# Optimization experiments

Hardware: AMD Instinct MI355X
Metric: run time of the kernel (lower is better)

## Reference

```python
import jax, jax.numpy as jnp
import numpy as np

L, K, C, D, E = 4, 3, 512, 512, 512   # layers, kwidth, channels, embed_dim, encoding_dim
T, B, S, V, MAXT = 1024, 16, 512, 32, 1024


def setup_inputs() -> dict:
    key = jax.random.key(0)
    ks = jax.random.split(key, 16)
    n = lambda k, sh, s=0.02: jax.random.normal(k, sh, dtype=jnp.float32) * s
    return {
        "labels": jax.random.randint(ks[0], (T, B), 0, V),
        "enc_seq": jax.random.uniform(ks[1], (S, B, E), dtype=jnp.float32),
        "label_embed_W": n(ks[2], (V, D)),
        "time_embed_W": n(ks[3], (MAXT, D)),
        "conv_glu_w": n(ks[4], (L, C, C, K)),
        "conv_glu_b": jnp.zeros((L, C), jnp.float32),
        "conv_id_w": n(ks[5], (L, C, C, K)),
        "conv_id_b": jnp.zeros((L, C), jnp.float32),
        "res_proj_w": n(ks[6], (L, C, C)),
        "res_proj_b": jnp.zeros((L, C), jnp.float32),
        "inres_w": n(ks[7], (L, C, D)),
        "inres_b": jnp.zeros((L, C), jnp.float32),
        "in2enc_w": n(ks[8], (L, E, C)),
        "in2enc_b": jnp.ones((L, E), jnp.float32),  # positive bias keeps sum-normalizer well conditioned
        "lab2enc_w": n(ks[9], (L, E, D)),
        "lab2enc_b": jnp.zeros((L, E), jnp.float32),
        "enc2in_w": n(ks[10], (L, C, E)),
        "enc2in_b": jnp.zeros((L, C), jnp.float32),
        "out_res_w": n(ks[11], (V, D)),
        "out_res_b": jnp.zeros((V,), jnp.float32),
        "out_proj_w": n(ks[12], (V, C)),
        "out_proj_b": jnp.zeros((V,), jnp.float32),
    }


def causal_conv(x, w, b):
    # x: (T, B, Cin); w: (Cout, Cin, K) -> left-padded (causal) conv, out (T, B, Cout)
    x_ = jnp.transpose(x, (1, 2, 0))  # (B, Cin, T)
    y = jax.lax.conv_general_dilated(
        x_, w, window_strides=(1,), padding=[(w.shape[-1] - 1, 0)],
        dimension_numbers=("NCH", "OIH", "NCH"))
    return jnp.transpose(y, (2, 0, 1)) + b


def reference(labels, enc_seq, label_embed_W, time_embed_W, conv_glu_w, conv_glu_b,
              conv_id_w, conv_id_b, res_proj_w, res_proj_b, inres_w, inres_b,
              in2enc_w, in2enc_b, lab2enc_w, lab2enc_b, enc2in_w, enc2in_b,
              out_res_w, out_res_b, out_proj_w, out_proj_b):
    Tn = labels.shape[0]
    emb = label_embed_W[labels] + time_embed_W[jnp.arange(Tn)][:, None, :]  # (T,B,D)
    h = emb
    for i in range(conv_glu_w.shape[0]):
        x = causal_conv(h, conv_glu_w[i], conv_glu_b[i])
        g = causal_conv(h, conv_id_w[i], conv_id_b[i])
        conv_out = (x * jax.nn.sigmoid(g)
                    + jnp.einsum('tbc,oc->tbo', h, res_proj_w[i]) + res_proj_b[i])
        # attention: dot-product scores normalized by their SUM over encoder axis (no softmax)
        d = (jnp.einsum('tbc,ec->tbe', conv_out, in2enc_w[i]) + in2enc_b[i]
             + jnp.einsum('tbd,ed->tbe', emb, lab2enc_w[i]) + lab2enc_b[i])
        raw = jnp.einsum('tbe,sbe->tsb', d, enc_seq)          # (T,S,B)
        attn = raw / jnp.sum(raw, axis=1, keepdims=True)
        ctx = jnp.einsum('tsb,sbe->tbe', attn, enc_seq)        # (T,B,E)
        ctx_proj = jnp.einsum('tbe,ce->tbc', ctx, enc2in_w[i]) + enc2in_b[i]
        h = conv_out + ctx_proj + jnp.einsum('tbd,cd->tbc', emb, inres_w[i]) + inres_b[i]
    out = (jnp.einsum('tbc,vc->tbv', h, out_proj_w) + out_proj_b
           + jnp.einsum('tbd,vd->tbv', emb, out_res_w) + out_res_b)
    return out
```

## Files before the change

### kernel.cpp

```cpp
#include <hip/hip_runtime.h>
#include <math.h>

#define Tn 1024
#define Bn 16
#define Sn 512
#define Vn 32
#define Cn 512
#define En 512
#define Ln 4
#define Kw 3
#define MROWS 16384
#define PADROWS 32
#define PADE (PADROWS * Cn)

typedef short bf16x8 __attribute__((ext_vector_type(8)));
typedef float f32x4 __attribute__((ext_vector_type(4)));

__device__ __forceinline__ unsigned short cvt_bf16(float x) {
  unsigned u = __builtin_bit_cast(unsigned, x);
  u = (u + 0x7FFFu + ((u >> 16) & 1u)) >> 16;
  return (unsigned short)u;
}
__device__ __forceinline__ float bf2f(unsigned short h) {
  unsigned u = ((unsigned)h) << 16;
  return __builtin_bit_cast(float, u);
}

#define GL16(g, l)                                                                     \
  __builtin_amdgcn_global_load_lds((const __attribute__((address_space(1))) void*)(g), \
                                   (__attribute__((address_space(3))) void*)(l), 16, 0, 0)

template <int N>
__device__ __forceinline__ void wait_vm_bar() {
  asm volatile("s_waitcnt vmcnt(%0)\n\ts_barrier" ::"i"(N) : "memory");
}
__device__ __forceinline__ void tail_bar() {
  asm volatile("s_waitcnt lgkmcnt(0)\n\ts_barrier" ::: "memory");
}
#define VMB(N)                                               \
  do {                                                       \
    asm volatile("s_waitcnt vmcnt(%0)" ::"i"(N) : "memory"); \
    __builtin_amdgcn_s_barrier();                            \
  } while (0)

__device__ __forceinline__ const unsigned short* seg_sel(const unsigned short* s0,
                                                         const unsigned short* s1,
                                                         const unsigned short* s2, int q) {
  const unsigned short* r = s0;
  r = (q == 1) ? s1 : r;
  r = (q == 2) ? s2 : r;
  return r;
}

template <int EPI, int NKT>
__global__ __launch_bounds__(512, 4) void g2(
    const unsigned short* __restrict__ a0, const unsigned short* __restrict__ a1,
    const unsigned short* __restrict__ a2, int ald, size_t az,
    const unsigned short* __restrict__ b0, const unsigned short* __restrict__ b1,
    const unsigned short* __restrict__ b2, int bld, size_t bz,
    const float* __restrict__ bias, const float* __restrict__ dden,
    unsigned short* __restrict__ out, int old_, size_t oz) {
  __shared__ char SA[32768], SB[32768];
  const int tid = threadIdx.x;
  const int lane = tid & 63, wave = tid >> 6;
  const int r15 = lane & 15;
  const int sq = ((lane >> 4) ^ ((r15 >> 1) & 3)) << 4;
  const int waveM = (wave >> 2) << 6;
  const int waveN = (wave & 3) << 5;
  const int m0 = blockIdx.x * 128, n0 = blockIdx.y * 128;
  const int z = blockIdx.z;
  const unsigned short* A0 = a0 + (size_t)z * az;
  const unsigned short* A1 = a1 + (size_t)z * az;
  const unsigned short* A2 = a2 + (size_t)z * az;
  const unsigned short* B0 = b0 + (size_t)z * bz;
  const unsigned short* B1 = b1 + (size_t)z * bz;
  const unsigned short* B2 = b2 + (size_t)z * bz;
  const int strow = tid >> 2;
  const int stcol = ((tid & 3) ^ ((tid >> 3) & 3)) << 3;
  const int lofs = tid * 16;
  f32x4 acc[4][2] = {};

#define STAGE_T(KT, SL)                                                               \
  do {                                                                                \
    const unsigned short* ab_ = seg_sel(A0, A1, A2, (KT) >> 3) +                      \
                                (size_t)(m0 + strow) * ald + (((KT)&7) << 6) + stcol; \
    const unsigned short* bb_ = seg_sel(B0, B1, B2, (KT) >> 3) +                      \
                                (size_t)(n0 + strow) * bld + (((KT)&7) << 6) + stcol; \
    GL16(ab_, SA + (SL)*16384 + lofs);                                                \
    GL16(ab_ + 32, SA + (SL)*16384 + 8192 + lofs);                                    \
    GL16(bb_, SB + (SL)*16384 + lofs);                                                \
    GL16(bb_ + 32, SB + (SL)*16384 + 8192 + lofs);                                    \
  } while (0)

  STAGE_T(0, 0);
  for (int kt = 0; kt < NKT; ++kt) {
    const int sl = kt & 1;
    if (kt + 1 < NKT) {
      STAGE_T(kt + 1, sl ^ 1);
      wait_vm_bar<4>();
    } else {
      wait_vm_bar<0>();
    }
    const char* abase = SA + sl * 16384 + (waveM + r15) * 64 + sq;
    const char* bbase = SB + sl * 16384 + (waveN + r15) * 64 + sq;
    __builtin_amdgcn_s_setprio(1);
#pragma unroll
    for (int kp = 0; kp < 2; ++kp) {
      bf16x8 af[4], bfv[2];
#pragma unroll
      for (int i = 0; i < 4; ++i) af[i] = *(const bf16x8*)(abase + kp * 8192 + i * 1024);
#pragma unroll
      for (int j = 0; j < 2; ++j) bfv[j] = *(const bf16x8*)(bbase + kp * 8192 + j * 1024);
#pragma unroll
      for (int i = 0; i < 4; ++i)
#pragma unroll
        for (int j = 0; j < 2; ++j)
          acc[i][j] = __builtin_amdgcn_mfma_f32_16x16x32_bf16(af[i], bfv[j], acc[i][j], 0, 0, 0);
    }
    __builtin_amdgcn_s_setprio(0);
    tail_bar();
  }
#undef STAGE_T

  const int q4 = (lane >> 4) << 2;
#pragma unroll
  for (int i = 0; i < 4; ++i) {
    int row = m0 + waveM + i * 16 + q4;
    if constexpr (EPI == 0) {
      int xcol = ((n0 + waveN) >> 1) + r15;
      float bx = bias[n0 + waveN + r15];
      float bg = bias[n0 + waveN + 16 + r15];
#pragma unroll
      for (int rr = 0; rr < 4; ++rr) {
        float xv = acc[i][0][rr] + bx;
        float gv = acc[i][1][rr] + bg;
        float sg = 1.f / (1.f + __expf(-gv));
        out[(size_t)(row + rr) * 512 + xcol] = cvt_bf16(xv * sg);
      }
    } else if constexpr (EPI == 3) {
#pragma unroll
      for (int rr = 0; rr < 4; ++rr) {
        float inv = 1.f / dden[z + (size_t)(row + rr) * 16];
#pragma unroll
        for (int j = 0; j < 2; ++j) {
          int col = n0 + waveN + j * 16 + r15;
          out[(size_t)z * oz + (size_t)(row + rr) * old_ + col] = cvt_bf16(acc[i][j][rr] * inv);
        }
      }
    } else {
#pragma unroll
      for (int j = 0; j < 2; ++j) {
        int col = n0 + waveN + j * 16 + r15;
#pragma unroll
        for (int rr = 0; rr < 4; ++rr) {
          size_t o = (size_t)z * oz + (size_t)(row + rr) * old_ + col;
          out[o] = cvt_bf16(acc[i][j][rr]);
        }
      }
    }
  }
}

template <int EPI>
__global__ __launch_bounds__(512, 2) void g3t(
    const unsigned short* __restrict__ a0, const unsigned short* __restrict__ a1,
    const unsigned short* __restrict__ a2, const unsigned short* __restrict__ b0,
    const unsigned short* __restrict__ b1, const unsigned short* __restrict__ b2,
    const float* __restrict__ bias, const unsigned short* __restrict__ addbf,
    unsigned short* __restrict__ out) {
  __shared__ char LA[2][32768];
  __shared__ char LB[2][16384];
  const int tid = threadIdx.x;
  const int lane = tid & 63;
  const int wm = (tid >> 6) >> 1;
  const int wn = (tid >> 6) & 1;
  const int r15 = lane & 15;
  const int l4 = lane >> 4;
  const int q4 = l4 << 2;
  const int m0 = blockIdx.x * 256, n0 = blockIdx.y * 128;
  const int srow = tid >> 3;
  const int scol = (((tid & 7) ^ (srow & 7)) << 3);
  const int sdst = tid << 4;
  f32x4 acc[4][4] = {};
  bf16x8 afr[4][2], b01[2][2], b23[2][2];

#define TGA(KT, BB)                                                                \
  do {                                                                             \
    const unsigned short* s_ = seg_sel(a0, a1, a2, (KT) >> 3) +                    \
                               (size_t)(m0 + srow) * 512 + (((KT)&7) << 6) + scol; \
    GL16(s_, LA[BB] + sdst);                                                       \
    GL16(s_ + (size_t)64 * 512, LA[BB] + 8192 + sdst);                             \
    GL16(s_ + (size_t)128 * 512, LA[BB] + 16384 + sdst);                           \
    GL16(s_ + (size_t)192 * 512, LA[BB] + 24576 + sdst);                           \
  } while (0)
#define TGB(KT, BB)                                                                \
  do {                                                                             \
    const unsigned short* s_ = seg_sel(b0, b1, b2, (KT) >> 3) +                    \
                               (size_t)(n0 + srow) * 512 + (((KT)&7) << 6) + scol; \
    GL16(s_, LB[BB] + sdst);                                                       \
    GL16(s_ + (size_t)64 * 512, LB[BB] + 8192 + sdst);                             \
  } while (0)
#define TRA(SL)                                                                            \
  do {                                                                                     \
    _Pragma("unroll") for (int f = 0; f < 4; ++f) _Pragma("unroll") for (int kp = 0;       \
                                                                         kp < 2; ++kp) {  \
      int ar = ((f >> 1) << 7) + (wm << 5) + ((f & 1) << 4) + r15;                         \
      afr[f][kp] =                                                                         \
          *(const bf16x8*)(LA[SL] + ar * 128 + ((((kp << 2) | l4) ^ (ar & 7)) << 4));      \
    }                                                                                      \
  } while (0)
#define TRB(SL, CH, DST)                                                                   \
  do {                                                                                     \
    _Pragma("unroll") for (int c = 0; c < 2; ++c) _Pragma("unroll") for (int kp = 0;       \
                                                                         kp < 2; ++kp) {  \
      int br = ((CH) << 6) + (wn << 5) + (c << 4) + r15;                                   \
      DST[c][kp] =                                                                         \
          *(const bf16x8*)(LB[SL] + br * 128 + ((((kp << 2) | l4) ^ (br & 7)) << 4));      \
    }                                                                                      \
  } while (0)
#define MMT(BF, C0)                                                                        \
  do {                                                                                     \
    __builtin_amdgcn_s_setprio(1);                                                         \
    _Pragma("unroll") for (int f = 0; f < 4; ++f) _Pragma("unroll") for (int c = 0; c < 2; \
                                                                         ++c)             \
        _Pragma("unroll") for (int kp = 0; kp < 2; ++kp) acc[f][(C0) + c] =                \
            __builtin_amdgcn_mfma_f32_16x16x32_bf16(afr[f][kp], BF[c][kp],                 \
                                                    acc[f][(C0) + c], 0, 0, 0);            \
    __builtin_amdgcn_s_setprio(0);                                                         \
  } while (0)
#define TGRP(KT, W1, W2, STG)              \
  do {                                     \
    const int sl_ = (KT)&1, sn_ = sl_ ^ 1; \
    if (STG) TGA((KT) + 1, sn_);           \
    VMB(W1);                               \
    TRA(sl_);                              \
    TRB(sl_, 0, b01);                      \
    MMT(b01, 0);                           \
    if (STG) TGB((KT) + 1, sn_);           \
    VMB(W2);                               \
    TRB(sl_, 1, b23);                      \
    MMT(b23, 2);                           \
  } while (0)

  TGA(0, 0);
  TGB(0, 0);
  for (int kt = 0; kt < 23; ++kt) TGRP(kt, 5, 6, 1);
  TGRP(23, 1, 0, 0);
#undef TGRP

#pragma unroll
  for (int f = 0; f < 4; ++f) {
    int grow = m0 + ((f >> 1) << 7) + (wm << 5) + ((f & 1) << 4) + q4;
#pragma unroll
    for (int c = 0; c < 4; ++c) {
      int gcol = n0 + ((c >> 1) << 6) + (wn << 5) + ((c & 1) << 4) + r15;
      float bb = bias[gcol];
#pragma unroll
      for (int rr = 0; rr < 4; ++rr) {
        size_t o = (size_t)(grow + rr) * 512 + gcol;
        float v = acc[f][c][rr] + bb;
        if constexpr (EPI == 2) v += bf2f(addbf[o]);
        out[o] = cvt_bf16(v);
      }
    }
  }
}

__global__ __launch_bounds__(256) void den_kernel(const unsigned short* __restrict__ d,
                                                  const float* __restrict__ Esum,
                                                  float* __restrict__ den) {
  int gtid = blockIdx.x * 256 + threadIdx.x;
  int row = gtid >> 6;
  int lane = threadIdx.x & 63;
  int b = row & 15;
  const unsigned short* dp = d + (size_t)row * 512 + lane * 8;
  const float* ep = Esum + b * 512 + lane * 8;
  float s = 0.f;
#pragma unroll
  for (int q = 0; q < 8; ++q) s += bf2f(dp[q]) * ep[q];
  for (int off = 32; off; off >>= 1) s += __shfl_down(s, off, 64);
  if (lane == 0) den[row] = s;
}

__global__ __launch_bounds__(256, 4) void k_outm(const unsigned short* __restrict__ hd,
                                                 const unsigned short* __restrict__ embd,
                                                 const unsigned short* __restrict__ wcat2,
                                                 const float* __restrict__ bcat2,
                                                 float* __restrict__ out) {
  __shared__ char SA[32768];
  __shared__ char SBo[8192];
  const int tid = threadIdx.x;
  const int lane = tid & 63, wave = tid >> 6;
  const int r15 = lane & 15;
  const int sq = ((lane >> 4) ^ ((r15 >> 1) & 3)) << 4;
  const int waveM = wave << 5;
  const int m0 = blockIdx.x * 128;
  f32x4 acc[2][2] = {};

#define OSTAGE(KT, SL)                                                                   \
  do {                                                                                   \
    const unsigned short* aseg = ((KT) < 8) ? hd : embd;                                 \
    int kc = ((KT)&7) << 6;                                                              \
    _Pragma("unroll") for (int q = 0; q < 2; ++q) {                                      \
      int unit = q * 256 + tid;                                                          \
      int row = unit >> 2, chunk = unit & 3;                                             \
      int swc = chunk ^ ((row >> 1) & 3);                                                \
      GL16(aseg + (size_t)(m0 + row) * 512 + kc + swc * 8, SA + (SL)*16384 + unit * 16); \
      GL16(aseg + (size_t)(m0 + row) * 512 + kc + 32 + swc * 8,                          \
           SA + (SL)*16384 + 8192 + unit * 16);                                          \
    }                                                                                    \
    {                                                                                    \
      int half = tid >> 7;                                                               \
      int u = tid & 127;                                                                 \
      int row = u >> 2, chunk = u & 3;                                                   \
      int swc = chunk ^ ((row >> 1) & 3);                                                \
      GL16(wcat2 + (size_t)row * 1024 + ((KT) << 6) + half * 32 + swc * 8,               \
           SBo + (SL)*4096 + half * 2048 + u * 16);                                      \
    }                                                                                    \
  } while (0)

  OSTAGE(0, 0);
  for (int kt = 0; kt < 16; ++kt) {
    const int sl = kt & 1;
    if (kt + 1 < 16) {
      OSTAGE(kt + 1, sl ^ 1);
      wait_vm_bar<5>();
    } else {
      wait_vm_bar<0>();
    }
    const char* abase = SA + sl * 16384 + (waveM + r15) * 64 + sq;
    const char* bbase = SBo + sl * 4096 + r15 * 64 + sq;
    __builtin_amdgcn_s_setprio(1);
#pragma unroll
    for (int kp = 0; kp < 2; ++kp) {
      bf16x8 af[2], bfv[2];
#pragma unroll
      for (int i = 0; i < 2; ++i) af[i] = *(const bf16x8*)(abase + kp * 8192 + i * 1024);
#pragma unroll
      for (int j = 0; j < 2; ++j) bfv[j] = *(const bf16x8*)(bbase + kp * 2048 + j * 1024);
#pragma unroll
      for (int i = 0; i < 2; ++i)
#pragma unroll
        for (int j = 0; j < 2; ++j)
          acc[i][j] = __builtin_amdgcn_mfma_f32_16x16x32_bf16(af[i], bfv[j], acc[i][j], 0, 0, 0);
    }
    __builtin_amdgcn_s_setprio(0);
    tail_bar();
  }
#undef OSTAGE

  const int q4 = (lane >> 4) << 2;
#pragma unroll
  for (int i = 0; i < 2; ++i) {
    int row = m0 + waveM + i * 16 + q4;
#pragma unroll
    for (int j = 0; j < 2; ++j) {
      int col = j * 16 + r15;
      float bb = bcat2[col];
#pragma unroll
      for (int rr = 0; rr < 4; ++rr) out[(size_t)(row + rr) * 32 + col] = acc[i][j][rr] + bb;
    }
  }
}


__global__ __launch_bounds__(256) void k_prep2(const int* __restrict__ labels,
                                               const float* __restrict__ labW,
                                               const float* __restrict__ timeW,
                                               unsigned short* __restrict__ embd,
                                               unsigned short* __restrict__ embp,
                                               unsigned short* __restrict__ h0p,
                                               unsigned short* __restrict__ h1p) {
  int idx = blockIdx.x * 256 + threadIdx.x;
  if (idx < MROWS * 512) {
    int dd = idx & 511;
    int m = idx >> 9;
    int t = m >> 4;
    embd[idx] = cvt_bf16(labW[labels[m] * 512 + dd] + timeW[t * 512 + dd]);
    return;
  }
  int i = idx - MROWS * 512;
  if (i < PADE) embp[i] = 0;
  else if (i < 2 * PADE) h0p[i - PADE] = 0;
  else h1p[i - 2 * PADE] = 0;
}

__global__ __launch_bounds__(256) void k_prep1(
    const float* __restrict__ res_proj_w, const float* __restrict__ in2enc_w,
    const float* __restrict__ lab2enc_w, const float* __restrict__ inres_w,
    const float* __restrict__ enc2in_w, const float* __restrict__ wx,
    const float* __restrict__ wg, const float* __restrict__ cbx, const float* __restrict__ cbg,
    const float* __restrict__ opw, const float* __restrict__ orw, const float* __restrict__ opb,
    const float* __restrict__ orb, unsigned short* __restrict__ wres,
    unsigned short* __restrict__ w_i2e, unsigned short* __restrict__ w_l2e,
    unsigned short* __restrict__ w_inr, unsigned short* __restrict__ w_e2i,
    unsigned short* __restrict__ wcat, float* __restrict__ bcat,
    unsigned short* __restrict__ wcat2, float* __restrict__ bcat2) {
  int idx = blockIdx.x * 256 + threadIdx.x;
  const int WNc = 1 << 20;
  if (idx < 5 * WNc) {
    int which = idx >> 20, i = idx & (WNc - 1);
    const float* s = (which == 0)   ? res_proj_w
                     : (which == 1) ? in2enc_w
                     : (which == 2) ? lab2enc_w
                     : (which == 3) ? inres_w
                                    : enc2in_w;
    unsigned short* d = (which == 0)   ? wres
                        : (which == 1) ? w_i2e
                        : (which == 2) ? w_l2e
                        : (which == 3) ? w_inr
                                       : w_e2i;
    d[i] = cvt_bf16(s[i]);
    return;
  }
  idx -= 5 * WNc;
  if (idx < Ln * 1024 * 1536) {
    int k = idx % 1536;
    int tmp = idx / 1536;
    int orow = tmp & 1023;
    int l = tmp >> 10;
    int tap = k >> 9, c = k & 511;
    int q = orow >> 5, r = orow & 31;
    int srow = q * 16 + (r & 15);
    const float* src = (r < 16) ? wx : wg;
    wcat[idx] = cvt_bf16(src[(((size_t)l * 512 + srow) * 512 + c) * 3 + tap]);
    return;
  }
  idx -= Ln * 1024 * 1536;
  if (idx < Ln * 1024) {
    int orow = idx & 1023, l = idx >> 10;
    int q = orow >> 5, r = orow & 31;
    bcat[idx] = (r < 16) ? cbx[l * 512 + q * 16 + r] : cbg[l * 512 + q * 16 + (r & 15)];
    return;
  }
  idx -= Ln * 1024;
  {
    int v = idx >> 10, k = idx & 1023;
    float val = (k < 512) ? opw[v * 512 + k] : orw[v * 512 + k - 512];
    wcat2[idx] = cvt_bf16(val);
    if (idx < 32) bcat2[idx] = opb[idx] + orb[idx];
  }
}

__global__ __launch_bounds__(256) void k_tr512(const float* __restrict__ w,
                                               unsigned short* __restrict__ wt) {
  __shared__ unsigned short t[64][65];
  int r0 = blockIdx.x * 64, c0 = blockIdx.y * 64;
  size_t base = (size_t)blockIdx.z * 512 * 512;
  int c = threadIdx.x & 63, rr = threadIdx.x >> 6;
#pragma unroll
  for (int i = 0; i < 16; ++i) {
    int r = rr + i * 4;
    t[r][c] = cvt_bf16(w[base + (size_t)(r0 + r) * 512 + c0 + c]);
  }
  __syncthreads();
#pragma unroll
  for (int i = 0; i < 16; ++i) {
    int r = rr + i * 4;
    wt[base + (size_t)(c0 + r) * 512 + r0 + c] = t[c][r];
  }
}

__global__ void esum_kernel(const float* __restrict__ enc, float* __restrict__ Esum) {
  int p = blockIdx.x * 256 + threadIdx.x;
  float s = 0.f;
  for (int ss = 0; ss < Sn; ++ss) s += enc[(size_t)ss * Bn * En + p];
  Esum[p] = s;
}

__global__ __launch_bounds__(256) void k_encT(const float* __restrict__ enc,
                                              unsigned short* __restrict__ encT) {
  __shared__ unsigned short t[64][66];
  int s0 = blockIdx.x * 64, e0 = blockIdx.y * 64, b = blockIdx.z;
  int c = threadIdx.x & 63, r0 = threadIdx.x >> 6;
#pragma unroll
  for (int i = 0; i < 16; ++i) {
    int r = r0 + i * 4;
    t[r][c] = cvt_bf16(enc[((size_t)(s0 + r) * Bn + b) * En + e0 + c]);
  }
  __syncthreads();
#pragma unroll
  for (int i = 0; i < 16; ++i) {
    int r = r0 + i * 4;
    encT[((size_t)b * En + e0 + r) * Sn + s0 + c] = t[c][r];
  }
}

__global__ void k_biasprep(const float* __restrict__ i2e, const float* __restrict__ res_b,
                           const float* __restrict__ in2enc_b, const float* __restrict__ lab2enc_b,
                           const float* __restrict__ e2i_b, const float* __restrict__ inres_b,
                           float* __restrict__ bd, float* __restrict__ bh) {
  int idx = blockIdx.x * 256 + threadIdx.x;
  int l = idx >> 9;
  float v = 0.f;
  const float* row = i2e + (size_t)idx * 512;
  const float* rb = res_b + l * 512;
  for (int c = 0; c < 512; ++c) v += row[c] * rb[c];
  bd[idx] = v + in2enc_b[idx] + lab2enc_b[idx];
  bh[idx] = res_b[idx] + e2i_b[idx] + inres_b[idx];
}


extern "C" void kernel_launch(void* const* d_in, const int* in_sizes, int n_in,
                              void* d_out, int out_size, void* d_ws, size_t ws_size,
                              hipStream_t stream) {
  const int* labels = (const int*)d_in[0];
  const float* enc = (const float*)d_in[1];
  const float* labW = (const float*)d_in[2];
  const float* timeW = (const float*)d_in[3];
  const float* conv_glu_w = (const float*)d_in[4];
  const float* conv_glu_b = (const float*)d_in[5];
  const float* conv_id_w = (const float*)d_in[6];
  const float* conv_id_b = (const float*)d_in[7];
  const float* res_proj_w = (const float*)d_in[8];
  const float* res_proj_b = (const float*)d_in[9];
  const float* inres_w = (const float*)d_in[10];
  const float* inres_b = (const float*)d_in[11];
  const float* in2enc_w = (const float*)d_in[12];
  const float* in2enc_b = (const float*)d_in[13];
  const float* lab2enc_w = (const float*)d_in[14];
  const float* lab2enc_b = (const float*)d_in[15];
  const float* enc2in_w = (const float*)d_in[16];
  const float* enc2in_b = (const float*)d_in[17];
  const float* out_res_w = (const float*)d_in[18];
  const float* out_res_b = (const float*)d_in[19];
  const float* out_proj_w = (const float*)d_in[20];
  const float* out_proj_b = (const float*)d_in[21];
  float* out = (float*)d_out;

  char* cur = (char*)d_ws;
  auto alloc = [&](size_t bytes) {
    char* p = cur;
    cur += (bytes + 255) & ~(size_t)255;
    return p;
  };
  const size_t BIG = (size_t)MROWS * 512;
  const size_t WN = (size_t)Ln * Cn * Cn;
  const size_t ZL = (size_t)512 * 512;
  float* den = (float*)alloc(MROWS * 4);
  float* EsumB = (float*)alloc(Bn * En * 4);
  float* bd = (float*)alloc(Ln * 512 * 4);
  float* bh = (float*)alloc(Ln * 512 * 4);
  float* bcat = (float*)alloc(Ln * 1024 * 4);
  float* bcat2 = (float*)alloc(32 * 4);
  unsigned short* embp = (unsigned short*)alloc((PADE + BIG) * 2);
  unsigned short* h0p = (unsigned short*)alloc((PADE + BIG) * 2);
  unsigned short* h1p = (unsigned short*)alloc((PADE + BIG) * 2);
  unsigned short* glubf = (unsigned short*)alloc(BIG * 2);
  unsigned short* dbf = (unsigned short*)alloc(BIG * 2);
  unsigned short* ctxbf = (unsigned short*)alloc(BIG * 2);
  unsigned short* encT = (unsigned short*)alloc((size_t)Bn * En * Sn * 2);
  unsigned short* Mbf = (unsigned short*)alloc((size_t)Bn * En * En * 2);
  unsigned short* wres = (unsigned short*)alloc(WN * 2);
  unsigned short* resT = (unsigned short*)alloc(WN * 2);
  unsigned short* wfuse = (unsigned short*)alloc(WN * 2);
  unsigned short* wcat = (unsigned short*)alloc((size_t)Ln * 1024 * 1536 * 2);
  unsigned short* wcat2 = (unsigned short*)alloc((size_t)32 * 1024 * 2);
  unsigned short* w_i2e = (unsigned short*)alloc(WN * 2);
  unsigned short* w_l2e = (unsigned short*)alloc(WN * 2);
  unsigned short* w_inr = (unsigned short*)alloc(WN * 2);
  unsigned short* w_e2i = (unsigned short*)alloc(WN * 2);

  unsigned short* embd = embp + PADE;
  unsigned short* h0d = h0p + PADE;
  unsigned short* h1d = h1p + PADE;

  k_prep2<<<(MROWS * 512 + 3 * PADE) / 256, 256, 0, stream>>>(labels, labW, timeW, embd, embp,
                                                              h0p, h1p);
  {
    int total = 5 * (1 << 20) + Ln * 1024 * 1536 + Ln * 1024 + 32 * 1024;
    k_prep1<<<total / 256, 256, 0, stream>>>(res_proj_w, in2enc_w, lab2enc_w, inres_w, enc2in_w,
                                             conv_glu_w, conv_id_w, conv_glu_b, conv_id_b,
                                             out_proj_w, out_res_w, out_proj_b, out_res_b, wres,
                                             w_i2e, w_l2e, w_inr, w_e2i, wcat, bcat, wcat2,
                                             bcat2);
  }
  k_tr512<<<dim3(8, 8, Ln), 256, 0, stream>>>(res_proj_w, resT);
  esum_kernel<<<Bn * En / 256, 256, 0, stream>>>(enc, EsumB);
  k_biasprep<<<Ln * 512 / 256, 256, 0, stream>>>(in2enc_w, res_proj_b, in2enc_b, lab2enc_b,
                                                 enc2in_b, inres_b, bd, bh);
  k_encT<<<dim3(Sn / 64, En / 64, Bn), 256, 0, stream>>>(enc, encT);
  g2<4, 8><<<dim3(4, 4, Bn), 512, 0, stream>>>(encT, encT, encT, Sn, ZL, encT, encT, encT, Sn,
                                               ZL, nullptr, nullptr, Mbf, 512, ZL);
  g2<4, 8><<<dim3(4, 4, Ln), 512, 0, stream>>>(w_i2e, w_i2e, w_i2e, 512, ZL, resT, resT, resT,
                                               512, ZL, nullptr, nullptr, wfuse, 512, ZL);

  const unsigned short* hdata = embd;
  unsigned short* hbufs[2] = {h0d, h1d};
  for (int l = 0; l < Ln; ++l) {
    const size_t wo = (size_t)l * Cn * Cn;
    const unsigned short* wc = wcat + (size_t)l * 1024 * 1536;
    g2<0, 24><<<dim3(128, 8), 512, 0, stream>>>(hdata - 2 * Bn * 512, hdata - Bn * 512, hdata,
                                                512, 0, wc, wc + 512, wc + 1024, 1536, 0,
                                                bcat + l * 1024, nullptr, glubf, 512, 0);
    g3t<1><<<dim3(64, 4), 512, 0, stream>>>(glubf, hdata, embd, w_i2e + wo, wfuse + wo,
                                            w_l2e + wo, bd + l * 512, nullptr, dbf);
    den_kernel<<<MROWS / 4, 256, 0, stream>>>(dbf, EsumB, den);
    g2<3, 8><<<dim3(8, 4, Bn), 512, 0, stream>>>(dbf, dbf, dbf, 8192, 512, Mbf, Mbf, Mbf, 512,
                                                 ZL, nullptr, den, ctxbf, 8192, 512);
    g3t<2><<<dim3(64, 4), 512, 0, stream>>>(hdata, ctxbf, embd, wres + wo, w_e2i + wo,
                                            w_inr + wo, bh + l * 512, glubf, hbufs[l & 1]);
    hdata = hbufs[l & 1];
  }

  k_outm<<<MROWS / 128, 256, 0, stream>>>(hdata, embd, wcat2, bcat2, out);
}
```

Before: 672.5 us.

## Fuse causal conv taps into one K-loop sharing a haloed activation tile

Result: no change. 679.3 us (+1.0%).

```diff
diff --git a/kernel.cpp b/kernel.cpp
--- a/kernel.cpp
+++ b/kernel.cpp
@@ -10,7 +10,7 @@
 #define Ln 4
 #define Kw 3
 #define MROWS 16384
-#define PADROWS 32
+#define PADROWS 64
 #define PADE (PADROWS * Cn)
 
 typedef short bf16x8 __attribute__((ext_vector_type(8)));
@@ -50,6 +50,99 @@
   r = (q == 1) ? s1 : r;
   r = (q == 2) ? s2 : r;
   return r;
+}
+
+__global__ __launch_bounds__(512, 2) void gfglu(const unsigned short* __restrict__ hd,
+                                                const unsigned short* __restrict__ wc,
+                                                const float* __restrict__ bias,
+                                                unsigned short* __restrict__ out) {
+  __shared__ char LS[2][73728];
+  const int tid = threadIdx.x;
+  const int lane = tid & 63, wave = tid >> 6;
+  const int r15 = lane & 15;
+  const int l4 = lane >> 4;
+  const int q4 = l4 << 2;
+  const int waveM = (wave >> 2) << 6;
+  const int waveN = (wave & 3) << 5;
+  const int m0 = blockIdx.x * 128, n0 = blockIdx.y * 128;
+  f32x4 acc[4][2] = {};
+
+#define GFSTAGE(KT, SL)                                                        \
+  do {                                                                         \
+    _Pragma("unroll") for (int j = 0; j < 3; ++j) {                            \
+      int u = j * 512 + tid;                                                   \
+      int row = u >> 3;                                                        \
+      int sw = ((u & 7) ^ (row & 7)) << 3;                                     \
+      GL16(hd + (ptrdiff_t)(m0 - 64 + row) * 512 + (KT) * 64 + sw,             \
+           LS[SL] + u * 16);                                                   \
+    }                                                                          \
+    _Pragma("unroll") for (int j = 0; j < 6; ++j) {                            \
+      int u = j * 512 + tid;                                                   \
+      int row = u >> 3;                                                        \
+      int tap = row >> 7, wr = row & 127;                                      \
+      int sw = ((u & 7) ^ (row & 7)) << 3;                                     \
+      GL16(wc + (size_t)(n0 + wr) * 1536 + tap * 512 + (KT) * 64 + sw,         \
+           LS[SL] + 24576 + u * 16);                                           \
+    }                                                                          \
+  } while (0)
+
+  GFSTAGE(0, 0);
+  for (int kt = 0; kt < 8; ++kt) {
+    const int sl = kt & 1;
+    if (kt < 7) {
+      GFSTAGE(kt + 1, sl ^ 1);
+      VMB(9);
+    } else {
+      VMB(0);
+    }
+    const char* Ab = (const char*)LS[sl];
+    const char* Bb = (const char*)LS[sl] + 24576;
+    __builtin_amdgcn_s_setprio(1);
+#pragma unroll
+    for (int t = 0; t < 3; ++t) {
+      bf16x8 af[4][2], bfv[2][2];
+#pragma unroll
+      for (int f = 0; f < 4; ++f)
+#pragma unroll
+        for (int kp = 0; kp < 2; ++kp) {
+          int ar = waveM + f * 16 + 16 * t + 32 + r15;
+          af[f][kp] = *(const bf16x8*)(Ab + ar * 128 + ((((kp << 2) | l4) ^ (ar & 7)) << 4));
+        }
+#pragma unroll
+      for (int c = 0; c < 2; ++c)
+#pragma unroll
+        for (int kp = 0; kp < 2; ++kp) {
+          int br = t * 128 + waveN + c * 16 + r15;
+          bfv[c][kp] = *(const bf16x8*)(Bb + br * 128 + ((((kp << 2) | l4) ^ (br & 7)) << 4));
+        }
+#pragma unroll
+      for (int f = 0; f < 4; ++f)
+#pragma unroll
+        for (int c = 0; c < 2; ++c)
+#pragma unroll
+          for (int kp = 0; kp < 2; ++kp)
+            acc[f][c] = __builtin_amdgcn_mfma_f32_16x16x32_bf16(af[f][kp], bfv[c][kp],
+                                                                acc[f][c], 0, 0, 0);
+    }
+    __builtin_amdgcn_s_setprio(0);
+    tail_bar();
+  }
+#undef GFSTAGE
+
+  const int xcol = ((n0 + waveN) >> 1) + r15;
+  const float bx = bias[n0 + waveN + r15];
+  const float bg = bias[n0 + waveN + 16 + r15];
+#pragma unroll
+  for (int f = 0; f < 4; ++f) {
+    int row = m0 + waveM + f * 16 + q4;
+#pragma unroll
+    for (int rr = 0; rr < 4; ++rr) {
+      float xv = acc[f][0][rr] + bx;
+      float gv = acc[f][1][rr] + bg;
+      float sg = 1.f / (1.f + __expf(-gv));
+      out[(size_t)(row + rr) * 512 + xcol] = cvt_bf16(xv * sg);
+    }
+  }
 }
 
 template <int EPI, int NKT>
@@ -126,18 +219,7 @@
 #pragma unroll
   for (int i = 0; i < 4; ++i) {
     int row = m0 + waveM + i * 16 + q4;
-    if constexpr (EPI == 0) {
-      int xcol = ((n0 + waveN) >> 1) + r15;
-      float bx = bias[n0 + waveN + r15];
-      float bg = bias[n0 + waveN + 16 + r15];
-#pragma unroll
-      for (int rr = 0; rr < 4; ++rr) {
-        float xv = acc[i][0][rr] + bx;
-        float gv = acc[i][1][rr] + bg;
-        float sg = 1.f / (1.f + __expf(-gv));
-        out[(size_t)(row + rr) * 512 + xcol] = cvt_bf16(xv * sg);
-      }
-    } else if constexpr (EPI == 3) {
+    if constexpr (EPI == 3) {
 #pragma unroll
       for (int rr = 0; rr < 4; ++rr) {
         float inv = 1.f / dden[z + (size_t)(row + rr) * 16];
@@ -273,11 +355,14 @@
   int row = gtid >> 6;
   int lane = threadIdx.x & 63;
   int b = row & 15;
-  const unsigned short* dp = d + (size_t)row * 512 + lane * 8;
+  bf16x8 v = *(const bf16x8*)(d + (size_t)row * 512 + lane * 8);
   const float* ep = Esum + b * 512 + lane * 8;
-  float s = 0.f;
-#pragma unroll
-  for (int q = 0; q < 8; ++q) s += bf2f(dp[q]) * ep[q];
+  float4 e0 = *(const float4*)(ep);
+  float4 e1 = *(const float4*)(ep + 4);
+  float s = bf2f((unsigned short)v[0]) * e0.x + bf2f((unsigned short)v[1]) * e0.y +
+            bf2f((unsigned short)v[2]) * e0.z + bf2f((unsigned short)v[3]) * e0.w +
+            bf2f((unsigned short)v[4]) * e1.x + bf2f((unsigned short)v[5]) * e1.y +
+            bf2f((unsigned short)v[6]) * e1.z + bf2f((unsigned short)v[7]) * e1.w;
   for (int off = 32; off; off >>= 1) s += __shfl_down(s, off, 64);
   if (lane == 0) den[row] = s;
 }
@@ -590,9 +675,7 @@
   for (int l = 0; l < Ln; ++l) {
     const size_t wo = (size_t)l * Cn * Cn;
     const unsigned short* wc = wcat + (size_t)l * 1024 * 1536;
-    g2<0, 24><<<dim3(128, 8), 512, 0, stream>>>(hdata - 2 * Bn * 512, hdata - Bn * 512, hdata,
-                                                512, 0, wc, wc + 512, wc + 1024, 1536, 0,
-                                                bcat + l * 1024, nullptr, glubf, 512, 0);
+    gfglu<<<dim3(128, 8), 512, 0, stream>>>(hdata, wc, bcat + l * 1024, glubf);
     g3t<1><<<dim3(64, 4), 512, 0, stream>>>(glubf, hdata, embd, w_i2e + wo, wfuse + wo,
                                             w_l2e + wo, bd + l * 512, nullptr, dbf);
     den_kernel<<<MROWS / 4, 256, 0, stream>>>(dbf, EsumB, den);
```
